# Performance work log

Measured on AMD Instinct MI355X. Metric: run time of the kernel, lower is better.

## Reference

```python
import jax, jax.numpy as jnp
import numpy as np

B, H, S, D = 2, 8, 2048, 64
WINDOW = 3            # local_attention_window (default in torch forward)
FRAC = 0.3            # percentage_frac hardcoded in create_window_tensor call
MASK_FILL = -1.0e9


def window_kernel(window, frac):
    # create_window_tensor: [ (1-f)^n ... (1-f)^1, 1, (1-f)^1 ... (1-f)^n ]
    n = (window - 1) // 2
    side = np.array([(1.0 - frac) ** i for i in range(n, 0, -1)], dtype=np.float32)
    vals = np.concatenate([side, np.array([1.0], np.float32), side[::-1]])
    return jnp.asarray(vals)


def setup_inputs() -> dict:
    key = jax.random.key(0)
    kq, kk, kv = jax.random.split(key, 3)
    queries = jax.random.normal(kq, (B, H, S, D), jnp.float32)
    keys = jax.random.normal(kk, (B, H, S, D), jnp.float32)
    values = jax.random.normal(kv, (B, H, S, D), jnp.float32)
    # causal mask: True positions are filled with -1e9 (masked_fill semantics)
    mask = jnp.triu(jnp.ones((S, S), dtype=bool), 1)[None, None]  # [1,1,S,S]
    # linear_bias: nn.Parameter(torch.zeros(Sk)) created inside forward
    beta = jnp.zeros((S,), jnp.float32)
    return {"queries": queries, "keys": keys, "values": values,
            "beta": beta, "mask": mask}


def reference(queries, keys, values, beta, mask):
    d = keys.shape[-1]
    # scores = Q K^T / sqrt(d)
    scores = jnp.einsum("bhqd,bhkd->bhqk", queries, keys) / jnp.sqrt(
        jnp.asarray(d, queries.dtype))
    scores = jnp.where(mask, jnp.asarray(MASK_FILL, scores.dtype), scores)
    # include_local_attention=True, local_attention_dim_vertical=False:
    # the torch code transposes, conv2d with a [1,W] kernel along the last
    # axis, transposes back -> 1D cross-correlation along the QUERY axis.
    # Kernel is symmetric so correlation == convolution. Zero padding.
    kern = window_kernel(WINDOW, FRAC)
    p = (WINDOW - 1) // 2
    xp = jnp.pad(scores, ((0, 0), (0, 0), (p, p), (0, 0)))
    Sq = scores.shape[2]
    scores = sum(kern[i] * jax.lax.dynamic_slice_in_dim(xp, i, Sq, axis=2)
                 for i in range(WINDOW))
    # linear_bias=True: add zero-initialized per-key-position bias
    scores = scores + beta  # broadcasts over last dim [Sk]
    weights = jax.nn.softmax(scores, axis=-1)
    return jnp.einsum("bhqk,bhkd->bhqd", weights, values)
```

## Files before the change

kernel.cpp:

```cpp
#include <hip/hip_runtime.h>


typedef short bf16x8 __attribute__((ext_vector_type(8)));
typedef float f32x4  __attribute__((ext_vector_type(4)));

constexpr int S_ = 2048;
constexpr int D_ = 64;
constexpr float LOG2E = 1.44269504088896341f;
constexpr float KSC = 0.125f * LOG2E;

__device__ __forceinline__ unsigned pk2(float lo, float hi) {
    union { float f; unsigned u; } a, b;
    a.f = lo; b.f = hi;
    return __builtin_amdgcn_perm(b.u + 0x8000u, a.u + 0x8000u, 0x07060302u);
}

__global__ __launch_bounds__(256)
void cvt8(const float* __restrict__ K, const float* __restrict__ V,
          unsigned short* __restrict__ F)
{
    __shared__ float T[64][68];

    const int bid = blockIdx.x;
    const int hd = bid & 15, tt = bid >> 4;
    const float* Kt = K + ((size_t)hd * S_ + tt * 64) * D_;
    const float* Vt = V + ((size_t)hd * S_ + tt * 64) * D_;
    unsigned short* Ft = F + (size_t)(hd * 32 + tt) * 8192;

    const int t = threadIdx.x;
    const int key = t >> 2, d0 = (t & 3) << 4;

    {
        const float* vp = Vt + key * D_ + d0;
        #pragma unroll
        for (int i = 0; i < 4; ++i) {
            float4 v4 = *(const float4*)(vp + 4 * i);
            T[d0 + 4 * i + 0][key] = v4.x;
            T[d0 + 4 * i + 1][key] = v4.y;
            T[d0 + 4 * i + 2][key] = v4.z;
            T[d0 + 4 * i + 3][key] = v4.w;
        }
    }

    {
        const float* kp = Kt + key * D_ + d0;
        float4 a = *(const float4*)(kp);
        float4 b = *(const float4*)(kp + 4);
        float4 c = *(const float4*)(kp + 8);
        float4 d = *(const float4*)(kp + 12);
        uint4 w0 = make_uint4(pk2(a.x, a.y), pk2(a.z, a.w), pk2(b.x, b.y), pk2(b.z, b.w));
        uint4 w1 = make_uint4(pk2(c.x, c.y), pk2(c.z, c.w), pk2(d.x, d.y), pk2(d.z, d.w));
        const int r5 = key & 31;
        const int kh = key >> 5, mb = (r5 >> 2) & 1;
        const int n = ((r5 >> 3) << 2) | (r5 & 3);
        const int hh = d0 >> 5, qd0 = (d0 >> 3) & 3;
        const int f0 = (kh << 2) | (mb << 1) | hh;
        *(uint4*)(Ft + f0 * 512 + ((qd0 << 4) | n) * 8)       = w0;
        *(uint4*)(Ft + f0 * 512 + (((qd0 + 1) << 4) | n) * 8) = w1;
    }
    __syncthreads();

    #pragma unroll
    for (int s = 0; s < 2; ++s) {
        const int slot = t + s * 256;
        const int fr = slot >> 6, lane = slot & 63;
        const int kh = fr >> 2, mb = fr & 3, n = lane & 15, qd = lane >> 4;
        const float* row = &T[mb * 16 + n][kh * 32 + qd * 8];
        uint4 w = make_uint4(pk2(row[0], row[1]), pk2(row[2], row[3]),
                             pk2(row[4], row[5]), pk2(row[6], row[7]));
        *(uint4*)(Ft + (8 + fr) * 512 + lane * 8) = w;
    }
}

#define LD_T(TILE, KA, VB) do {                                              \
    const unsigned short* fp_ = Fh + (size_t)(TILE) * 8192;                  \
    KA[0][0] = *(const bf16x8*)(fp_ + kfo[0][0]);                            \
    KA[0][1] = *(const bf16x8*)(fp_ + kfo[0][1]);                            \
    KA[1][0] = *(const bf16x8*)(fp_ + kfo[1][0]);                            \
    KA[1][1] = *(const bf16x8*)(fp_ + kfo[1][1]);                            \
    VB[0] = *(const bf16x8*)(fp_ + vfo[0]);                                  \
    VB[1] = *(const bf16x8*)(fp_ + vfo[1]);                                  \
    VB[2] = *(const bf16x8*)(fp_ + vfo[2]);                                  \
    VB[3] = *(const bf16x8*)(fp_ + vfo[3]);                                  \
} while (0)

#define COMP_T(TILE, KA, VB) do {                                            \
    const int kb_ = ((TILE) << 6) + kvo;                                     \
    const float4 b0_ = *(const float4*)&bl[kb_];                             \
    const float4 b1_ = *(const float4*)&bl[kb_ + 4];                         \
    const float bt_[8] = {b0_.x, b0_.y, b0_.z, b0_.w,                        \
                          b1_.x, b1_.y, b1_.z, b1_.w};                       \
    const f32x4 zz_ = {0, 0, 0, 0};                                          \
    f32x4 acc_[2][2];                                                        \
    acc_[0][0] = __builtin_amdgcn_mfma_f32_16x16x32_bf16(KA[0][1], qb[0][1], \
        __builtin_amdgcn_mfma_f32_16x16x32_bf16(KA[0][0], qb[0][0], zz_, 0, 0, 0), 0, 0, 0); \
    acc_[0][1] = __builtin_amdgcn_mfma_f32_16x16x32_bf16(KA[0][1], qb[1][1], \
        __builtin_amdgcn_mfma_f32_16x16x32_bf16(KA[0][0], qb[1][0], zz_, 0, 0, 0), 0, 0, 0); \
    acc_[1][0] = __builtin_amdgcn_mfma_f32_16x16x32_bf16(KA[1][1], qb[0][1], \
        __builtin_amdgcn_mfma_f32_16x16x32_bf16(KA[1][0], qb[0][0], zz_, 0, 0, 0), 0, 0, 0); \
    acc_[1][1] = __builtin_amdgcn_mfma_f32_16x16x32_bf16(KA[1][1], qb[1][1], \
        __builtin_amdgcn_mfma_f32_16x16x32_bf16(KA[1][0], qb[1][0], zz_, 0, 0, 0), 0, 0, 0); \
    const bool dm_ = (TILE) == nt - 1;                                       \
    _Pragma("unroll")                                                        \
    for (int ng_ = 0; ng_ < 2; ++ng_) {                                      \
        const int qr_ = qbase + (ng_ << 4) + n_l;                            \
        float pv_[8];                                                        \
        float la_ = 0.0f;                                                    \
        _Pragma("unroll")                                                    \
        for (int jj_ = 0; jj_ < 8; ++jj_) {                                  \
            float sv_ = fmaf(acc_[jj_ >> 2][ng_][jj_ & 3], KSC, bt_[jj_]);   \
            if (dm_) {                                                       \
                const int key_ = kb_ + jj_;                                  \
                if (!((key_ < qr_) || (qr_ == 0 && key_ == 0))) sv_ = -1.0e30f; \
            }                                                                \
            pv_[jj_] = __builtin_amdgcn_exp2f(sv_);                          \
            la_ += pv_[jj_];                                                 \
        }                                                                    \
        l[ng_] += la_;                                                       \
        union { unsigned u[4]; bf16x8 v; } pf_;                              \
        pf_.u[0] = pk2(pv_[0], pv_[1]);                                      \
        pf_.u[1] = pk2(pv_[2], pv_[3]);                                      \
        pf_.u[2] = pk2(pv_[4], pv_[5]);                                      \
        pf_.u[3] = pk2(pv_[6], pv_[7]);                                      \
        o[0][ng_] = __builtin_amdgcn_mfma_f32_16x16x32_bf16(VB[0], pf_.v, o[0][ng_], 0, 0, 0); \
        o[1][ng_] = __builtin_amdgcn_mfma_f32_16x16x32_bf16(VB[1], pf_.v, o[1][ng_], 0, 0, 0); \
        o[2][ng_] = __builtin_amdgcn_mfma_f32_16x16x32_bf16(VB[2], pf_.v, o[2][ng_], 0, 0, 0); \
        o[3][ng_] = __builtin_amdgcn_mfma_f32_16x16x32_bf16(VB[3], pf_.v, o[3][ng_], 0, 0, 0); \
    }                                                                        \
} while (0)

__global__ __launch_bounds__(512, 2)
void attn16(const float* __restrict__ Q, const float* __restrict__ beta,
            const unsigned short* __restrict__ F, float* __restrict__ out)
{
    __shared__ float slab[2][64][72];
    __shared__ float bl[S_];

    const int bid = blockIdx.x;
    const int hd = bid & 15;
    const int pr = bid >> 4;

    const float* Qh = Q + (size_t)hd * S_ * D_;
    const unsigned short* Fh = F + (size_t)hd * 32 * 8192;

    const int t = threadIdx.x, lane = t & 63;
    const int wv = t >> 6;
    const int kh = wv & 1, par = (wv >> 1) & 1, qh = wv >> 2;
    const int n_l = lane & 15, qd = lane >> 4;

    #pragma unroll
    for (int i = 0; i < 4; ++i) bl[t + i * 512] = beta[t + i * 512] * LOG2E;
    __syncthreads();

    const int lo = lane * 8;
    int kfo[2][2], vfo[4];
    #pragma unroll
    for (int mb = 0; mb < 2; ++mb)
        #pragma unroll
        for (int hh = 0; hh < 2; ++hh)
            kfo[mb][hh] = ((kh << 2) | (mb << 1) | hh) * 512 + lo;
    #pragma unroll
    for (int mb = 0; mb < 4; ++mb)
        vfo[mb] = (8 + (kh << 2) + mb) * 512 + lo;

    const int kvo = (kh << 5) + (qd << 3);

    for (int p = 0; p < 2; ++p) {
        const int j = p ? (31 - pr) : pr;
        const int q0 = j << 6;
        const int nt = j + 1;
        const int qbase = q0 + (qh << 5);

        bf16x8 qb[2][2];
        #pragma unroll
        for (int ng = 0; ng < 2; ++ng) {
            const int q = qbase + (ng << 4) + n_l;
            const float wp = (q > 0) ? 0.7f : 0.0f;
            const float wn = (q + 1 < S_) ? 0.7f : 0.0f;
            const float* qc = Qh + (size_t)q * D_;
            const float* qpp = qc - ((q > 0) ? D_ : 0);
            const float* qnn = qc + ((q + 1 < S_) ? D_ : 0);
            #pragma unroll
            for (int hh = 0; hh < 2; ++hh) {
                const int d0 = (hh << 5) + (qd << 3);
                float4 c0 = *(const float4*)(qc + d0),  c1 = *(const float4*)(qc + d0 + 4);
                float4 p0 = *(const float4*)(qpp + d0), p1 = *(const float4*)(qpp + d0 + 4);
                float4 n0 = *(const float4*)(qnn + d0), n1 = *(const float4*)(qnn + d0 + 4);
                float e0 = fmaf(wn, n0.x, fmaf(wp, p0.x, c0.x));
                float e1 = fmaf(wn, n0.y, fmaf(wp, p0.y, c0.y));
                float e2 = fmaf(wn, n0.z, fmaf(wp, p0.z, c0.z));
                float e3 = fmaf(wn, n0.w, fmaf(wp, p0.w, c0.w));
                float e4 = fmaf(wn, n1.x, fmaf(wp, p1.x, c1.x));
                float e5 = fmaf(wn, n1.y, fmaf(wp, p1.y, c1.y));
                float e6 = fmaf(wn, n1.z, fmaf(wp, p1.z, c1.z));
                float e7 = fmaf(wn, n1.w, fmaf(wp, p1.w, c1.w));
                union { unsigned u[4]; bf16x8 v; } qu;
                qu.u[0] = pk2(e0, e1); qu.u[1] = pk2(e2, e3);
                qu.u[2] = pk2(e4, e5); qu.u[3] = pk2(e6, e7);
                qb[ng][hh] = qu.v;
            }
        }

        f32x4 o[4][2];
        float l[2] = {0.0f, 0.0f};
        #pragma unroll
        for (int mb = 0; mb < 4; ++mb)
            #pragma unroll
            for (int ng = 0; ng < 2; ++ng) o[mb][ng] = (f32x4){0, 0, 0, 0};

        bf16x8 kaA[2][2], vbA[4];
        bf16x8 kaB[2][2], vbB[4];
        int it = par;
        if (it < nt) {
            LD_T(it, kaA, vbA);
            if (it + 2 < nt) LD_T(it + 2, kaB, vbB);
            while (it + 4 < nt) {
                COMP_T(it, kaA, vbA);
                LD_T(it + 4, kaA, vbA);
                COMP_T(it + 2, kaB, vbB);
                if (it + 6 < nt) LD_T(it + 6, kaB, vbB);
                it += 4;
            }
            COMP_T(it, kaA, vbA);
            if (it + 2 < nt) COMP_T(it + 2, kaB, vbB);
        }

        #pragma unroll
        for (int ng = 0; ng < 2; ++ng) {
            l[ng] += __shfl_xor(l[ng], 16);
            l[ng] += __shfl_xor(l[ng], 32);
        }
        __syncthreads();
        if (par == 1) {
            #pragma unroll
            for (int ng = 0; ng < 2; ++ng) {
                const int row = (qh << 5) + (ng << 4) + n_l;
                #pragma unroll
                for (int mb = 0; mb < 4; ++mb)
                    *(float4*)&slab[kh][row][(mb << 4) + (qd << 2)] =
                        make_float4(o[mb][ng][0], o[mb][ng][1], o[mb][ng][2], o[mb][ng][3]);
                if (qd == 0) slab[kh][row][64] = l[ng];
            }
        }
        __syncthreads();
        if (par == 0) {
            #pragma unroll
            for (int ng = 0; ng < 2; ++ng) {
                const int row = (qh << 5) + (ng << 4) + n_l;
                #pragma unroll
                for (int mb = 0; mb < 4; ++mb) {
                    float4 pv4 = *(float4*)&slab[kh][row][(mb << 4) + (qd << 2)];
                    o[mb][ng][0] += pv4.x; o[mb][ng][1] += pv4.y;
                    o[mb][ng][2] += pv4.z; o[mb][ng][3] += pv4.w;
                }
                l[ng] += slab[kh][row][64];
                if (kh == 0) {
                    #pragma unroll
                    for (int mb = 0; mb < 4; ++mb)
                        *(float4*)&slab[0][row][(mb << 4) + (qd << 2)] =
                            make_float4(o[mb][ng][0], o[mb][ng][1], o[mb][ng][2], o[mb][ng][3]);
                    if (qd == 0) slab[0][row][64] = l[ng];
                }
            }
        }
        __syncthreads();
        if (par == 0 && kh == 1) {
            #pragma unroll
            for (int ng = 0; ng < 2; ++ng) {
                const int row = (qh << 5) + (ng << 4) + n_l;
                const float inv = 1.0f / (l[ng] + slab[0][row][64]);
                float* op = out + ((size_t)hd * S_ + q0 + row) * D_ + (qd << 2);
                #pragma unroll
                for (int mb = 0; mb < 4; ++mb) {
                    float4 pv4 = *(float4*)&slab[0][row][(mb << 4) + (qd << 2)];
                    *(float4*)(op + (mb << 4)) =
                        make_float4((o[mb][ng][0] + pv4.x) * inv, (o[mb][ng][1] + pv4.y) * inv,
                                    (o[mb][ng][2] + pv4.z) * inv, (o[mb][ng][3] + pv4.w) * inv);
                }
            }
        }
    }
}

#undef LD_T
#undef COMP_T

extern "C" void kernel_launch(void* const* d_in, const int* in_sizes, int n_in,
                              void* d_out, int out_size, void* d_ws, size_t ws_size,
                              hipStream_t stream) {
    const float* Q    = (const float*)d_in[0];
    const float* K    = (const float*)d_in[1];
    const float* V    = (const float*)d_in[2];
    const float* beta = (const float*)d_in[3];
    float* out = (float*)d_out;

    unsigned short* F = (unsigned short*)d_ws;

    cvt8<<<dim3(512), 256, 0, stream>>>(K, V, F);
    attn16<<<dim3(256), 512, 0, stream>>>(Q, beta, F, out);
}
```

Before: 113.9 us.

## Launch one block per query tile and cut register prefetch depth for occupancy

Each block now handles a single 64-row query tile, with the grid doubled to 512 and heavy tiles scheduled first, instead of pairing a light and a heavy tile per block. The double-buffered K/V register prefetch is replaced by a single K prefetch, with V loaded inside the compute step. Launch bounds move to four blocks per CU. The aim is higher occupancy and better load balance across CUs to hide latency, at the cost of less software prefetch and possible register spilling under the tighter bound.

Measured after the change: 115.3 us. Within noise of the previous version (+1.3%).

```diff
diff --git a/kernel.cpp b/kernel.cpp
--- a/kernel.cpp
+++ b/kernel.cpp
@@ -72,20 +72,21 @@
     }
 }
 
-#define LD_T(TILE, KA, VB) do {                                              \
+#define LD_KA(TILE, KA) do {                                                 \
+    const unsigned short* fq_ = Fh + (size_t)(TILE) * 8192;                  \
+    KA[0][0] = *(const bf16x8*)(fq_ + kfo[0][0]);                            \
+    KA[0][1] = *(const bf16x8*)(fq_ + kfo[0][1]);                            \
+    KA[1][0] = *(const bf16x8*)(fq_ + kfo[1][0]);                            \
+    KA[1][1] = *(const bf16x8*)(fq_ + kfo[1][1]);                            \
+} while (0)
+
+#define COMP_T(TILE, KA, PRE) do {                                           \
+    const int kb_ = ((TILE) << 6) + kvo;                                     \
     const unsigned short* fp_ = Fh + (size_t)(TILE) * 8192;                  \
-    KA[0][0] = *(const bf16x8*)(fp_ + kfo[0][0]);                            \
-    KA[0][1] = *(const bf16x8*)(fp_ + kfo[0][1]);                            \
-    KA[1][0] = *(const bf16x8*)(fp_ + kfo[1][0]);                            \
-    KA[1][1] = *(const bf16x8*)(fp_ + kfo[1][1]);                            \
-    VB[0] = *(const bf16x8*)(fp_ + vfo[0]);                                  \
-    VB[1] = *(const bf16x8*)(fp_ + vfo[1]);                                  \
-    VB[2] = *(const bf16x8*)(fp_ + vfo[2]);                                  \
-    VB[3] = *(const bf16x8*)(fp_ + vfo[3]);                                  \
-} while (0)
-
-#define COMP_T(TILE, KA, VB) do {                                            \
-    const int kb_ = ((TILE) << 6) + kvo;                                     \
+    const bf16x8 vb0_ = *(const bf16x8*)(fp_ + vfo[0]);                      \
+    const bf16x8 vb1_ = *(const bf16x8*)(fp_ + vfo[1]);                      \
+    const bf16x8 vb2_ = *(const bf16x8*)(fp_ + vfo[2]);                      \
+    const bf16x8 vb3_ = *(const bf16x8*)(fp_ + vfo[3]);                      \
     const float4 b0_ = *(const float4*)&bl[kb_];                             \
     const float4 b1_ = *(const float4*)&bl[kb_ + 4];                         \
     const float bt_[8] = {b0_.x, b0_.y, b0_.z, b0_.w,                        \
@@ -100,6 +101,7 @@
         __builtin_amdgcn_mfma_f32_16x16x32_bf16(KA[1][0], qb[0][0], zz_, 0, 0, 0), 0, 0, 0); \
     acc_[1][1] = __builtin_amdgcn_mfma_f32_16x16x32_bf16(KA[1][1], qb[1][1], \
         __builtin_amdgcn_mfma_f32_16x16x32_bf16(KA[1][0], qb[1][0], zz_, 0, 0, 0), 0, 0, 0); \
+    PRE;                                                                     \
     const bool dm_ = (TILE) == nt - 1;                                       \
     _Pragma("unroll")                                                        \
     for (int ng_ = 0; ng_ < 2; ++ng_) {                                      \
@@ -122,15 +124,15 @@
         pf_.u[1] = pk2(pv_[2], pv_[3]);                                      \
         pf_.u[2] = pk2(pv_[4], pv_[5]);                                      \
         pf_.u[3] = pk2(pv_[6], pv_[7]);                                      \
-        o[0][ng_] = __builtin_amdgcn_mfma_f32_16x16x32_bf16(VB[0], pf_.v, o[0][ng_], 0, 0, 0); \
-        o[1][ng_] = __builtin_amdgcn_mfma_f32_16x16x32_bf16(VB[1], pf_.v, o[1][ng_], 0, 0, 0); \
-        o[2][ng_] = __builtin_amdgcn_mfma_f32_16x16x32_bf16(VB[2], pf_.v, o[2][ng_], 0, 0, 0); \
-        o[3][ng_] = __builtin_amdgcn_mfma_f32_16x16x32_bf16(VB[3], pf_.v, o[3][ng_], 0, 0, 0); \
+        o[0][ng_] = __builtin_amdgcn_mfma_f32_16x16x32_bf16(vb0_, pf_.v, o[0][ng_], 0, 0, 0); \
+        o[1][ng_] = __builtin_amdgcn_mfma_f32_16x16x32_bf16(vb1_, pf_.v, o[1][ng_], 0, 0, 0); \
+        o[2][ng_] = __builtin_amdgcn_mfma_f32_16x16x32_bf16(vb2_, pf_.v, o[2][ng_], 0, 0, 0); \
+        o[3][ng_] = __builtin_amdgcn_mfma_f32_16x16x32_bf16(vb3_, pf_.v, o[3][ng_], 0, 0, 0); \
     }                                                                        \
 } while (0)
 
-__global__ __launch_bounds__(512, 2)
-void attn16(const float* __restrict__ Q, const float* __restrict__ beta,
+__global__ __launch_bounds__(512, 4)
+void attn17(const float* __restrict__ Q, const float* __restrict__ beta,
             const unsigned short* __restrict__ F, float* __restrict__ out)
 {
     __shared__ float slab[2][64][72];
@@ -138,7 +140,11 @@
 
     const int bid = blockIdx.x;
     const int hd = bid & 15;
-    const int pr = bid >> 4;
+    const int rest = bid >> 4;
+    const int j = (rest < 16) ? (31 - 2 * rest) : (2 * (rest - 16));
+
+    const int q0 = j << 6;
+    const int nt = j + 1;
 
     const float* Qh = Q + (size_t)hd * S_ * D_;
     const unsigned short* Fh = F + (size_t)hd * 32 * 8192;
@@ -147,6 +153,7 @@
     const int wv = t >> 6;
     const int kh = wv & 1, par = (wv >> 1) & 1, qh = wv >> 2;
     const int n_l = lane & 15, qd = lane >> 4;
+    const int qbase = q0 + (qh << 5);
 
     #pragma unroll
     for (int i = 0; i < 4; ++i) bl[t + i * 512] = beta[t + i * 512] * LOG2E;
@@ -165,124 +172,109 @@
 
     const int kvo = (kh << 5) + (qd << 3);
 
-    for (int p = 0; p < 2; ++p) {
-        const int j = p ? (31 - pr) : pr;
-        const int q0 = j << 6;
-        const int nt = j + 1;
-        const int qbase = q0 + (qh << 5);
-
-        bf16x8 qb[2][2];
+    bf16x8 qb[2][2];
+    #pragma unroll
+    for (int ng = 0; ng < 2; ++ng) {
+        const int q = qbase + (ng << 4) + n_l;
+        const float wp = (q > 0) ? 0.7f : 0.0f;
+        const float wn = (q + 1 < S_) ? 0.7f : 0.0f;
+        const float* qc = Qh + (size_t)q * D_;
+        const float* qpp = qc - ((q > 0) ? D_ : 0);
+        const float* qnn = qc + ((q + 1 < S_) ? D_ : 0);
+        #pragma unroll
+        for (int hh = 0; hh < 2; ++hh) {
+            const int d0 = (hh << 5) + (qd << 3);
+            float4 c0 = *(const float4*)(qc + d0),  c1 = *(const float4*)(qc + d0 + 4);
+            float4 p0 = *(const float4*)(qpp + d0), p1 = *(const float4*)(qpp + d0 + 4);
+            float4 n0 = *(const float4*)(qnn + d0), n1 = *(const float4*)(qnn + d0 + 4);
+            float e0 = fmaf(wn, n0.x, fmaf(wp, p0.x, c0.x));
+            float e1 = fmaf(wn, n0.y, fmaf(wp, p0.y, c0.y));
+            float e2 = fmaf(wn, n0.z, fmaf(wp, p0.z, c0.z));
+            float e3 = fmaf(wn, n0.w, fmaf(wp, p0.w, c0.w));
+            float e4 = fmaf(wn, n1.x, fmaf(wp, p1.x, c1.x));
+            float e5 = fmaf(wn, n1.y, fmaf(wp, p1.y, c1.y));
+            float e6 = fmaf(wn, n1.z, fmaf(wp, p1.z, c1.z));
+            float e7 = fmaf(wn, n1.w, fmaf(wp, p1.w, c1.w));
+            union { unsigned u[4]; bf16x8 v; } qu;
+            qu.u[0] = pk2(e0, e1); qu.u[1] = pk2(e2, e3);
+            qu.u[2] = pk2(e4, e5); qu.u[3] = pk2(e6, e7);
+            qb[ng][hh] = qu.v;
+        }
+    }
+
+    f32x4 o[4][2];
+    float l[2] = {0.0f, 0.0f};
+    #pragma unroll
+    for (int mb = 0; mb < 4; ++mb)
+        #pragma unroll
+        for (int ng = 0; ng < 2; ++ng) o[mb][ng] = (f32x4){0, 0, 0, 0};
+
+    bf16x8 ka[2][2];
+    int it = par;
+    if (it < nt) {
+        LD_KA(it, ka);
+        for (; it + 2 < nt; it += 2) {
+            COMP_T(it, ka, LD_KA(it + 2, ka));
+        }
+        COMP_T(it, ka, (void)0);
+    }
+
+    #pragma unroll
+    for (int ng = 0; ng < 2; ++ng) {
+        l[ng] += __shfl_xor(l[ng], 16);
+        l[ng] += __shfl_xor(l[ng], 32);
+    }
+    if (par == 1) {
         #pragma unroll
         for (int ng = 0; ng < 2; ++ng) {
-            const int q = qbase + (ng << 4) + n_l;
-            const float wp = (q > 0) ? 0.7f : 0.0f;
-            const float wn = (q + 1 < S_) ? 0.7f : 0.0f;
-            const float* qc = Qh + (size_t)q * D_;
-            const float* qpp = qc - ((q > 0) ? D_ : 0);
-            const float* qnn = qc + ((q + 1 < S_) ? D_ : 0);
+            const int row = (qh << 5) + (ng << 4) + n_l;
             #pragma unroll
-            for (int hh = 0; hh < 2; ++hh) {
-                const int d0 = (hh << 5) + (qd << 3);
-                float4 c0 = *(const float4*)(qc + d0),  c1 = *(const float4*)(qc + d0 + 4);
-                float4 p0 = *(const float4*)(qpp + d0), p1 = *(const float4*)(qpp + d0 + 4);
-                float4 n0 = *(const float4*)(qnn + d0), n1 = *(const float4*)(qnn + d0 + 4);
-                float e0 = fmaf(wn, n0.x, fmaf(wp, p0.x, c0.x));
-                float e1 = fmaf(wn, n0.y, fmaf(wp, p0.y, c0.y));
-                float e2 = fmaf(wn, n0.z, fmaf(wp, p0.z, c0.z));
-                float e3 = fmaf(wn, n0.w, fmaf(wp, p0.w, c0.w));
-                float e4 = fmaf(wn, n1.x, fmaf(wp, p1.x, c1.x));
-                float e5 = fmaf(wn, n1.y, fmaf(wp, p1.y, c1.y));
-                float e6 = fmaf(wn, n1.z, fmaf(wp, p1.z, c1.z));
-                float e7 = fmaf(wn, n1.w, fmaf(wp, p1.w, c1.w));
-                union { unsigned u[4]; bf16x8 v; } qu;
-                qu.u[0] = pk2(e0, e1); qu.u[1] = pk2(e2, e3);
-                qu.u[2] = pk2(e4, e5); qu.u[3] = pk2(e6, e7);
-                qb[ng][hh] = qu.v;
+            for (int mb = 0; mb < 4; ++mb)
+                *(float4*)&slab[kh][row][(mb << 4) + (qd << 2)] =
+                    make_float4(o[mb][ng][0], o[mb][ng][1], o[mb][ng][2], o[mb][ng][3]);
+            if (qd == 0) slab[kh][row][64] = l[ng];
+        }
+    }
+    __syncthreads();
+    if (par == 0) {
+        #pragma unroll
+        for (int ng = 0; ng < 2; ++ng) {
+            const int row = (qh << 5) + (ng << 4) + n_l;
+            #pragma unroll
+            for (int mb = 0; mb < 4; ++mb) {
+                float4 pv4 = *(float4*)&slab[kh][row][(mb << 4) + (qd << 2)];
+                o[mb][ng][0] += pv4.x; o[mb][ng][1] += pv4.y;
+                o[mb][ng][2] += pv4.z; o[mb][ng][3] += pv4.w;
             }
-        }
-
-        f32x4 o[4][2];
-        float l[2] = {0.0f, 0.0f};
-        #pragma unroll
-        for (int mb = 0; mb < 4; ++mb)
-            #pragma unroll
-            for (int ng = 0; ng < 2; ++ng) o[mb][ng] = (f32x4){0, 0, 0, 0};
-
-        bf16x8 kaA[2][2], vbA[4];
-        bf16x8 kaB[2][2], vbB[4];
-        int it = par;
-        if (it < nt) {
-            LD_T(it, kaA, vbA);
-            if (it + 2 < nt) LD_T(it + 2, kaB, vbB);
-            while (it + 4 < nt) {
-                COMP_T(it, kaA, vbA);
-                LD_T(it + 4, kaA, vbA);
-                COMP_T(it + 2, kaB, vbB);
-                if (it + 6 < nt) LD_T(it + 6, kaB, vbB);
-                it += 4;
-            }
-            COMP_T(it, kaA, vbA);
-            if (it + 2 < nt) COMP_T(it + 2, kaB, vbB);
-        }
-
-        #pragma unroll
-        for (int ng = 0; ng < 2; ++ng) {
-            l[ng] += __shfl_xor(l[ng], 16);
-            l[ng] += __shfl_xor(l[ng], 32);
-        }
-        __syncthreads();
-        if (par == 1) {
-            #pragma unroll
-            for (int ng = 0; ng < 2; ++ng) {
-                const int row = (qh << 5) + (ng << 4) + n_l;
+            l[ng] += slab[kh][row][64];
+            if (kh == 0) {
                 #pragma unroll
                 for (int mb = 0; mb < 4; ++mb)
-                    *(float4*)&slab[kh][row][(mb << 4) + (qd << 2)] =
+                    *(float4*)&slab[0][row][(mb << 4) + (qd << 2)] =
                         make_float4(o[mb][ng][0], o[mb][ng][1], o[mb][ng][2], o[mb][ng][3]);
-                if (qd == 0) slab[kh][row][64] = l[ng];
+                if (qd == 0) slab[0][row][64] = l[ng];
             }
         }
-        __syncthreads();
-        if (par == 0) {
+    }
+    __syncthreads();
+    if (par == 0 && kh == 1) {
+        #pragma unroll
+        for (int ng = 0; ng < 2; ++ng) {
+            const int row = (qh << 5) + (ng << 4) + n_l;
+            const float inv = 1.0f / (l[ng] + slab[0][row][64]);
+            float* op = out + ((size_t)hd * S_ + q0 + row) * D_ + (qd << 2);
             #pragma unroll
-            for (int ng = 0; ng < 2; ++ng) {
-                const int row = (qh << 5) + (ng << 4) + n_l;
-                #pragma unroll
-                for (int mb = 0; mb < 4; ++mb) {
-                    float4 pv4 = *(float4*)&slab[kh][row][(mb << 4) + (qd << 2)];
-                    o[mb][ng][0] += pv4.x; o[mb][ng][1] += pv4.y;
-                    o[mb][ng][2] += pv4.z; o[mb][ng][3] += pv4.w;
-                }
-                l[ng] += slab[kh][row][64];
-                if (kh == 0) {
-                    #pragma unroll
-                    for (int mb = 0; mb < 4; ++mb)
-                        *(float4*)&slab[0][row][(mb << 4) + (qd << 2)] =
-                            make_float4(o[mb][ng][0], o[mb][ng][1], o[mb][ng][2], o[mb][ng][3]);
-                    if (qd == 0) slab[0][row][64] = l[ng];
-                }
+            for (int mb = 0; mb < 4; ++mb) {
+                float4 pv4 = *(float4*)&slab[0][row][(mb << 4) + (qd << 2)];
+                *(float4*)(op + (mb << 4)) =
+                    make_float4((o[mb][ng][0] + pv4.x) * inv, (o[mb][ng][1] + pv4.y) * inv,
+                                (o[mb][ng][2] + pv4.z) * inv, (o[mb][ng][3] + pv4.w) * inv);
             }
         }
-        __syncthreads();
-        if (par == 0 && kh == 1) {
-            #pragma unroll
-            for (int ng = 0; ng < 2; ++ng) {
-                const int row = (qh << 5) + (ng << 4) + n_l;
-                const float inv = 1.0f / (l[ng] + slab[0][row][64]);
-                float* op = out + ((size_t)hd * S_ + q0 + row) * D_ + (qd << 2);
-                #pragma unroll
-                for (int mb = 0; mb < 4; ++mb) {
-                    float4 pv4 = *(float4*)&slab[0][row][(mb << 4) + (qd << 2)];
-                    *(float4*)(op + (mb << 4)) =
-                        make_float4((o[mb][ng][0] + pv4.x) * inv, (o[mb][ng][1] + pv4.y) * inv,
-                                    (o[mb][ng][2] + pv4.z) * inv, (o[mb][ng][3] + pv4.w) * inv);
-                }
-            }
-        }
-    }
-}
-
-#undef LD_T
+    }
+}
+
+#undef LD_KA
 #undef COMP_T
 
 extern "C" void kernel_launch(void* const* d_in, const int* in_sizes, int n_in,
@@ -297,5 +289,5 @@
     unsigned short* F = (unsigned short*)d_ws;
 
     cvt8<<<dim3(512), 256, 0, stream>>>(K, V, F);
-    attn16<<<dim3(256), 512, 0, stream>>>(Q, beta, F, out);
-}
+    attn17<<<dim3(512), 512, 0, stream>>>(Q, beta, F, out);
+}
```

## Split key tiles across three wave parities with 768-thread blocks

Applied to the files above, without the earlier changes.

Raises the per-block wave count from 8 to 12 so each query/key-half pair gets three waves striding over key tiles instead of two. The reduction now sums two partial-output slabs into the parity-0 wave before the cross-key-half merge. The aim is more latency hiding and shorter per-wave key loops on the causal attention. In exchange it adds reduction traffic and LDS use, and the launch bound of 3 blocks per CU may squeeze registers.

After: 142.1 us. 1.25x slower.

```diff
diff --git a/kernel.cpp b/kernel.cpp
--- a/kernel.cpp
+++ b/kernel.cpp
@@ -129,11 +129,11 @@
     }                                                                        \
 } while (0)
 
-__global__ __launch_bounds__(512, 2)
-void attn16(const float* __restrict__ Q, const float* __restrict__ beta,
+__global__ __launch_bounds__(768, 3)
+void attn18(const float* __restrict__ Q, const float* __restrict__ beta,
             const unsigned short* __restrict__ F, float* __restrict__ out)
 {
-    __shared__ float slab[2][64][72];
+    __shared__ float slab[2][2][64][66];
     __shared__ float bl[S_];
 
     const int bid = blockIdx.x;
@@ -145,11 +145,16 @@
 
     const int t = threadIdx.x, lane = t & 63;
     const int wv = t >> 6;
-    const int kh = wv & 1, par = (wv >> 1) & 1, qh = wv >> 2;
+    const int kh = wv & 1;
+    const int rem = wv >> 1;
+    const int par = rem % 3, qh = rem / 3;
     const int n_l = lane & 15, qd = lane >> 4;
 
     #pragma unroll
-    for (int i = 0; i < 4; ++i) bl[t + i * 512] = beta[t + i * 512] * LOG2E;
+    for (int i = 0; i < 3; ++i) {
+        const int idx = t + i * 768;
+        if (idx < S_) bl[idx] = beta[idx] * LOG2E;
+    }
     __syncthreads();
 
     const int lo = lane * 8;
@@ -213,16 +218,16 @@
         int it = par;
         if (it < nt) {
             LD_T(it, kaA, vbA);
-            if (it + 2 < nt) LD_T(it + 2, kaB, vbB);
-            while (it + 4 < nt) {
+            if (it + 3 < nt) LD_T(it + 3, kaB, vbB);
+            while (it + 6 < nt) {
                 COMP_T(it, kaA, vbA);
-                LD_T(it + 4, kaA, vbA);
-                COMP_T(it + 2, kaB, vbB);
-                if (it + 6 < nt) LD_T(it + 6, kaB, vbB);
-                it += 4;
+                LD_T(it + 6, kaA, vbA);
+                COMP_T(it + 3, kaB, vbB);
+                if (it + 9 < nt) LD_T(it + 9, kaB, vbB);
+                it += 6;
             }
             COMP_T(it, kaA, vbA);
-            if (it + 2 < nt) COMP_T(it + 2, kaB, vbB);
+            if (it + 3 < nt) COMP_T(it + 3, kaB, vbB);
         }
 
         #pragma unroll
@@ -231,15 +236,16 @@
             l[ng] += __shfl_xor(l[ng], 32);
         }
         __syncthreads();
-        if (par == 1) {
+        if (par != 0) {
+            const int si = par - 1;
             #pragma unroll
             for (int ng = 0; ng < 2; ++ng) {
                 const int row = (qh << 5) + (ng << 4) + n_l;
                 #pragma unroll
                 for (int mb = 0; mb < 4; ++mb)
-                    *(float4*)&slab[kh][row][(mb << 4) + (qd << 2)] =
+                    *(float4*)&slab[kh][si][row][(mb << 4) + (qd << 2)] =
                         make_float4(o[mb][ng][0], o[mb][ng][1], o[mb][ng][2], o[mb][ng][3]);
-                if (qd == 0) slab[kh][row][64] = l[ng];
+                if (qd == 0) slab[kh][si][row][64] = l[ng];
             }
         }
         __syncthreads();
@@ -249,17 +255,20 @@
                 const int row = (qh << 5) + (ng << 4) + n_l;
                 #pragma unroll
                 for (int mb = 0; mb < 4; ++mb) {
-                    float4 pv4 = *(float4*)&slab[kh][row][(mb << 4) + (qd << 2)];
-                    o[mb][ng][0] += pv4.x; o[mb][ng][1] += pv4.y;
-                    o[mb][ng][2] += pv4.z; o[mb][ng][3] += pv4.w;
+                    #pragma unroll
+                    for (int si = 0; si < 2; ++si) {
+                        float4 pv4 = *(float4*)&slab[kh][si][row][(mb << 4) + (qd << 2)];
+                        o[mb][ng][0] += pv4.x; o[mb][ng][1] += pv4.y;
+                        o[mb][ng][2] += pv4.z; o[mb][ng][3] += pv4.w;
+                    }
                 }
-                l[ng] += slab[kh][row][64];
+                l[ng] += slab[kh][0][row][64] + slab[kh][1][row][64];
                 if (kh == 0) {
                     #pragma unroll
                     for (int mb = 0; mb < 4; ++mb)
-                        *(float4*)&slab[0][row][(mb << 4) + (qd << 2)] =
+                        *(float4*)&slab[0][0][row][(mb << 4) + (qd << 2)] =
                             make_float4(o[mb][ng][0], o[mb][ng][1], o[mb][ng][2], o[mb][ng][3]);
-                    if (qd == 0) slab[0][row][64] = l[ng];
+                    if (qd == 0) slab[0][0][row][64] = l[ng];
                 }
             }
         }
@@ -268,11 +277,11 @@
             #pragma unroll
             for (int ng = 0; ng < 2; ++ng) {
                 const int row = (qh << 5) + (ng << 4) + n_l;
-                const float inv = 1.0f / (l[ng] + slab[0][row][64]);
+                const float inv = 1.0f / (l[ng] + slab[0][0][row][64]);
                 float* op = out + ((size_t)hd * S_ + q0 + row) * D_ + (qd << 2);
                 #pragma unroll
                 for (int mb = 0; mb < 4; ++mb) {
-                    float4 pv4 = *(float4*)&slab[0][row][(mb << 4) + (qd << 2)];
+                    float4 pv4 = *(float4*)&slab[0][0][row][(mb << 4) + (qd << 2)];
                     *(float4*)(op + (mb << 4)) =
                         make_float4((o[mb][ng][0] + pv4.x) * inv, (o[mb][ng][1] + pv4.y) * inv,
                                     (o[mb][ng][2] + pv4.z) * inv, (o[mb][ng][3] + pv4.w) * inv);
@@ -297,5 +306,5 @@
     unsigned short* F = (unsigned short*)d_ws;
 
     cvt8<<<dim3(512), 256, 0, stream>>>(K, V, F);
-    attn16<<<dim3(256), 512, 0, stream>>>(Q, beta, F, out);
+    attn18<<<dim3(256), 768, 0, stream>>>(Q, beta, F, out);
 }
```
